# Performance work log

Hardware: AMD Instinct MI355X
Metric: run time of the kernel (lower is better)

The kernel has to match this reference:

```python
import jax, jax.numpy as jnp
import numpy as np

EPS = 1e-5


def _batchnorm(x, gamma, beta):
    # training-mode batch norm over the node axis, per feature channel
    mean = jnp.mean(x, axis=0)
    var = jnp.var(x, axis=0)  # biased variance, as torch uses for normalization
    return (x - mean) * jax.lax.rsqrt(var + EPS) * gamma + beta


def _gcn_conv(h, W, b, src, dst, norm, n_nodes):
    # h: [N, Fin] -> [N, Fout]; D^{-1/2}(A+I)D^{-1/2} (h W) + b
    h = h @ W                                   # [N, Fout]
    msgs = h[src] * norm[:, None]               # [E+N, Fout] gathered, normalized
    out = jax.ops.segment_sum(msgs, dst, num_segments=n_nodes)
    return out + b


def setup_inputs() -> dict:
    key = jax.random.key(0)
    ks = jax.random.split(key, 8)
    N, F, E, H = 50000, 512, 800000, 256
    inp = {
        "x": jax.random.normal(ks[0], (N, F), jnp.float32),
        "edge_index": jax.random.randint(ks[1], (2, E), 0, N, jnp.int64),
        "gamma1": jnp.ones((F,), jnp.float32),
        "beta1": jnp.zeros((F,), jnp.float32),
        "W1": jax.random.normal(ks[2], (F, H), jnp.float32) * (1.0 / np.sqrt(F)),
        "b1": jnp.zeros((H,), jnp.float32),
        "W2": jax.random.normal(ks[3], (H, H), jnp.float32) * (1.0 / np.sqrt(H)),
        "b2": jnp.zeros((H,), jnp.float32),
        "W3": jax.random.normal(ks[4], (H, H), jnp.float32) * (1.0 / np.sqrt(H)),
        "b3": jnp.zeros((H,), jnp.float32),
        "W4": jax.random.normal(ks[5], (H, H), jnp.float32) * (1.0 / np.sqrt(H)),
        "b4": jnp.zeros((H,), jnp.float32),
        "gamma2": jnp.ones((H,), jnp.float32),
        "beta2": jnp.zeros((H,), jnp.float32),
        "Wd": jax.random.normal(ks[6], (H, 5), jnp.float32) * (1.0 / np.sqrt(H)),
        "bd": jnp.zeros((5,), jnp.float32),
    }
    return inp


def reference(x, edge_index, gamma1, beta1, W1, b1, W2, b2, W3, b3, W4, b4,
              gamma2, beta2, Wd, bd):
    N = x.shape[0]
    loops = jnp.arange(N, dtype=edge_index.dtype)
    src = jnp.concatenate([edge_index[0], loops])
    dst = jnp.concatenate([edge_index[1], loops])
    deg = jax.ops.segment_sum(jnp.ones_like(src, dtype=x.dtype), dst, num_segments=N)
    dinv = jax.lax.rsqrt(deg)                    # deg >= 1 due to self-loops
    norm = dinv[src] * dinv[dst]                 # [E+N]

    h = _batchnorm(x, gamma1, beta1)
    h = _gcn_conv(h, W1, b1, src, dst, norm, N)
    h = _gcn_conv(h, W2, b2, src, dst, norm, N)
    h = _gcn_conv(h, W3, b3, src, dst, norm, N)
    h = _gcn_conv(h, W4, b4, src, dst, norm, N)
    h = _batchnorm(h, gamma2, beta2)
    # Flatten(start_dim=1) is identity on [N, 256]
    return jax.nn.sigmoid(h @ Wd + bd)           # [N, 5]
```

## Files before the change

kernel.cpp:

```cpp
#include <hip/hip_runtime.h>
#include <math.h>

#define BN_EPS 1e-5f

typedef float floatx4 __attribute__((ext_vector_type(4)));
typedef short shortx4 __attribute__((ext_vector_type(4)));
typedef short shortx8 __attribute__((ext_vector_type(8)));
typedef __bf16 bf16x8 __attribute__((ext_vector_type(8)));

__device__ __forceinline__ unsigned short f2b(float f) {
    unsigned int u = __builtin_bit_cast(unsigned int, f);
    u += 0x7fffu + ((u >> 16) & 1u);
    return (unsigned short)(u >> 16);
}
__device__ __forceinline__ float b2f(unsigned short s) {
    unsigned int u = ((unsigned int)s) << 16;
    return __builtin_bit_cast(float, u);
}
__device__ __forceinline__ float b2f_s(short s) { return b2f((unsigned short)s); }

__global__ __launch_bounds__(256)
void k_detect(const unsigned int* __restrict__ ei, int n_check, int* __restrict__ flag) {
    __shared__ int any;
    if (threadIdx.x == 0) any = 0;
    __syncthreads();
    for (int i = threadIdx.x; i < n_check; i += 256) {
        if (ei[2 * i + 1] != 0u) any = 1;
    }
    __syncthreads();
    if (threadIdx.x == 0) *flag = any;
}

__global__ __launch_bounds__(256)
void k_convert(const void* __restrict__ ei_raw, const int* __restrict__ flag,
               int* __restrict__ src, int* __restrict__ dst, int* __restrict__ cnt, int E) {
    int e = blockIdx.x * 256 + threadIdx.x;
    if (e >= E) return;
    int s, d;
    if (*flag) {
        const int* a = (const int*)ei_raw;
        s = a[e]; d = a[E + e];
    } else {
        const long long* a = (const long long*)ei_raw;
        s = (int)a[e]; d = (int)a[E + e];
    }
    src[e] = s;
    dst[e] = d;
    atomicAdd(&cnt[d], 1);
}

__global__ __launch_bounds__(1024)
void k_scan_sum(const int* __restrict__ cnt, int* __restrict__ bsum, int N) {
    __shared__ int s[1024];
    int i = blockIdx.x * 1024 + threadIdx.x;
    s[threadIdx.x] = (i < N) ? cnt[i] : 0;
    __syncthreads();
    for (int off = 512; off > 0; off >>= 1) {
        if (threadIdx.x < off) s[threadIdx.x] += s[threadIdx.x + off];
        __syncthreads();
    }
    if (threadIdx.x == 0) bsum[blockIdx.x] = s[0];
}

__global__ __launch_bounds__(1024)
void k_scan_part(int* __restrict__ bsum, int nb) {
    __shared__ int s[1024];
    int t = threadIdx.x;
    int v = (t < nb) ? bsum[t] : 0;
    s[t] = v;
    __syncthreads();
    for (int off = 1; off < 1024; off <<= 1) {
        int tmp = (t >= off) ? s[t - off] : 0;
        __syncthreads();
        s[t] += tmp;
        __syncthreads();
    }
    if (t < nb) bsum[t] = s[t] - v;
}

__global__ __launch_bounds__(1024)
void k_scan_final(const int* __restrict__ cnt, const int* __restrict__ bsum,
                  int* __restrict__ row_ptr, int* __restrict__ cursor,
                  float* __restrict__ dinv, int N) {
    __shared__ int s[1024];
    int b = blockIdx.x, t = threadIdx.x;
    int i = b * 1024 + t;
    int v = (i < N) ? cnt[i] : 0;
    s[t] = v;
    __syncthreads();
    for (int off = 1; off < 1024; off <<= 1) {
        int tmp = (t >= off) ? s[t - off] : 0;
        __syncthreads();
        s[t] += tmp;
        __syncthreads();
    }
    if (i < N) {
        int excl = bsum[b] + s[t] - v;
        row_ptr[i] = excl;
        cursor[i]  = excl;
        dinv[i] = rsqrtf((float)(v + 1));
        if (i == N - 1) row_ptr[N] = excl + v;
    }
}

__global__ __launch_bounds__(256)
void k_fill(const int* __restrict__ src, const int* __restrict__ dst,
            int* __restrict__ cursor, const float* __restrict__ dinv,
            int2* __restrict__ csr_sw, int E) {
    int e = blockIdx.x * 256 + threadIdx.x;
    if (e >= E) return;
    int s = src[e], d = dst[e];
    int p = atomicAdd(&cursor[d], 1);
    float w = dinv[s] * dinv[d];
    csr_sw[p] = make_int2(s, __builtin_bit_cast(int, w));
}

__global__ __launch_bounds__(256)
void k_bnstats_cast(const float* __restrict__ x, unsigned short* __restrict__ xb,
                    float* __restrict__ sum8, float* __restrict__ sumsq8, int N, int F) {
    __shared__ float ls[512], lq[512];
    int q   = F >> 2;
    int t   = threadIdx.x;
    int cq  = t % q;
    int ro  = t / q;
    int rpp = 256 / q;
    int step = gridDim.x * rpp;
    float s0 = 0.f, s1 = 0.f, s2 = 0.f, s3 = 0.f;
    float q0 = 0.f, q1 = 0.f, q2 = 0.f, q3 = 0.f;
    size_t colb = (size_t)cq * 4;
    for (int r = blockIdx.x * rpp + ro; r < N; r += 4 * step) {
        int rb = r + step, rc = r + 2 * step, rd = r + 3 * step;
        bool ob = rb < N, oc = rc < N, od = rd < N;
        float4 va = *(const float4*)&x[(size_t)r * F + colb];
        float4 vb, vc, vd;
        if (ob) vb = *(const float4*)&x[(size_t)rb * F + colb];
        if (oc) vc = *(const float4*)&x[(size_t)rc * F + colb];
        if (od) vd = *(const float4*)&x[(size_t)rd * F + colb];
        shortx4 o;
        o[0] = (short)f2b(va.x); o[1] = (short)f2b(va.y);
        o[2] = (short)f2b(va.z); o[3] = (short)f2b(va.w);
        *(shortx4*)&xb[(size_t)r * F + colb] = o;
        s0 += va.x; s1 += va.y; s2 += va.z; s3 += va.w;
        q0 += va.x * va.x; q1 += va.y * va.y; q2 += va.z * va.z; q3 += va.w * va.w;
        if (ob) {
            o[0] = (short)f2b(vb.x); o[1] = (short)f2b(vb.y);
            o[2] = (short)f2b(vb.z); o[3] = (short)f2b(vb.w);
            *(shortx4*)&xb[(size_t)rb * F + colb] = o;
            s0 += vb.x; s1 += vb.y; s2 += vb.z; s3 += vb.w;
            q0 += vb.x * vb.x; q1 += vb.y * vb.y; q2 += vb.z * vb.z; q3 += vb.w * vb.w;
        }
        if (oc) {
            o[0] = (short)f2b(vc.x); o[1] = (short)f2b(vc.y);
            o[2] = (short)f2b(vc.z); o[3] = (short)f2b(vc.w);
            *(shortx4*)&xb[(size_t)rc * F + colb] = o;
            s0 += vc.x; s1 += vc.y; s2 += vc.z; s3 += vc.w;
            q0 += vc.x * vc.x; q1 += vc.y * vc.y; q2 += vc.z * vc.z; q3 += vc.w * vc.w;
        }
        if (od) {
            o[0] = (short)f2b(vd.x); o[1] = (short)f2b(vd.y);
            o[2] = (short)f2b(vd.z); o[3] = (short)f2b(vd.w);
            *(shortx4*)&xb[(size_t)rd * F + colb] = o;
            s0 += vd.x; s1 += vd.y; s2 += vd.z; s3 += vd.w;
            q0 += vd.x * vd.x; q1 += vd.y * vd.y; q2 += vd.z * vd.z; q3 += vd.w * vd.w;
        }
    }
    for (int c = t; c < F; c += 256) { ls[c] = 0.f; lq[c] = 0.f; }
    __syncthreads();
    atomicAdd(&ls[cq * 4 + 0], s0); atomicAdd(&ls[cq * 4 + 1], s1);
    atomicAdd(&ls[cq * 4 + 2], s2); atomicAdd(&ls[cq * 4 + 3], s3);
    atomicAdd(&lq[cq * 4 + 0], q0); atomicAdd(&lq[cq * 4 + 1], q1);
    atomicAdd(&lq[cq * 4 + 2], q2); atomicAdd(&lq[cq * 4 + 3], q3);
    __syncthreads();
    int rep = (blockIdx.x & 7) * F;
    for (int c = t; c < F; c += 256) {
        atomicAdd(&sum8[rep + c],   ls[c]);
        atomicAdd(&sumsq8[rep + c], lq[c]);
    }
}

__global__ __launch_bounds__(256)
void k_bnstats_b(const unsigned short* __restrict__ x, float* __restrict__ sum,
                 float* __restrict__ sumsq, int N, int H) {
    __shared__ float ls[256], lq[256];
    int t  = threadIdx.x;
    int cg = t & 31;
    int ro = t >> 5;
    int step = gridDim.x * 8;
    float s[8], q[8];
    #pragma unroll
    for (int j = 0; j < 8; ++j) { s[j] = 0.f; q[j] = 0.f; }
    for (int r = blockIdx.x * 8 + ro; r < N; r += step) {
        shortx8 v = *(const shortx8*)&x[(size_t)r * H + cg * 8];
        #pragma unroll
        for (int j = 0; j < 8; ++j) {
            float f = b2f_s(v[j]);
            s[j] += f; q[j] += f * f;
        }
    }
    ls[t] = 0.f; lq[t] = 0.f;
    __syncthreads();
    #pragma unroll
    for (int j = 0; j < 8; ++j) {
        atomicAdd(&ls[cg * 8 + j], s[j]);
        atomicAdd(&lq[cg * 8 + j], q[j]);
    }
    __syncthreads();
    int rep = (blockIdx.x & 3) * H;
    atomicAdd(&sum[rep + t],   ls[t]);
    atomicAdd(&sumsq[rep + t], lq[t]);
}

__global__ __launch_bounds__(256)
void k_bnfin(const float* __restrict__ sum, const float* __restrict__ sumsq,
             const float* __restrict__ gamma, const float* __restrict__ beta,
             float* __restrict__ a, float* __restrict__ b, int N, int F, int nrep) {
    int c = blockIdx.x * 256 + threadIdx.x;
    if (c >= F) return;
    float s = 0.f, ss = 0.f;
    for (int i = 0; i < nrep; ++i) { s += sum[i * F + c]; ss += sumsq[i * F + c]; }
    float m   = s / (float)N;
    float var = ss / (float)N - m * m;
    float rs  = rsqrtf(var + BN_EPS);
    float aa  = gamma[c] * rs;
    a[c] = aa;
    b[c] = beta[c] - m * aa;
}

__global__ __launch_bounds__(256)
void k_castWT4(const float* __restrict__ W1, const float* __restrict__ W2,
               const float* __restrict__ W3, const float* __restrict__ W4,
               unsigned short* __restrict__ T1, unsigned short* __restrict__ T2,
               unsigned short* __restrict__ T3, unsigned short* __restrict__ T4,
               const float* __restrict__ bna, int F, int H) {
    int i = blockIdx.x * 256 + threadIdx.x;
    int n1 = F * H, n2 = H * H;
    if (i < n1) {
        int n = i / F, k = i % F;
        T1[i] = f2b(W1[(size_t)k * H + n] * bna[k]);
        return;
    }
    const float* W; unsigned short* T; int j;
    if (i < n1 + n2)          { W = W2; T = T2; j = i - n1; }
    else if (i < n1 + 2 * n2) { W = W3; T = T3; j = i - n1 - n2; }
    else if (i < n1 + 3 * n2) { W = W4; T = T4; j = i - n1 - 2 * n2; }
    else return;
    int n = j / H, k = j % H;
    T[j] = f2b(W[(size_t)k * H + n]);
}

__global__ __launch_bounds__(256)
void k_cvec(const float* __restrict__ W1, const float* __restrict__ bnb,
            float* __restrict__ cvec, int F, int H) {
    int j = threadIdx.x;
    int kslice = F / 8;
    int k0 = blockIdx.x * kslice;
    float s = 0.f;
    for (int k = k0; k < k0 + kslice; ++k)
        s += bnb[k] * W1[(size_t)k * H + j];
    atomicAdd(&cvec[j], s);
}

__device__ __forceinline__ void glds16(const void* g, void* l) {
    __builtin_amdgcn_global_load_lds(
        (const __attribute__((address_space(1))) unsigned int*)g,
        (__attribute__((address_space(3))) unsigned int*)l, 16, 0, 0);
}

__global__ __launch_bounds__(256)
void k_gemm_bf16(const unsigned short* __restrict__ A, const unsigned short* __restrict__ Bt,
                 unsigned short* __restrict__ C, int K, int NC) {
    __shared__ unsigned short As[128 * 32];
    __shared__ unsigned short Bs[128 * 32];
    int tid  = threadIdx.x;
    int wave = tid >> 6, lane = tid & 63;
    int row0 = blockIdx.x * 128;
    int col0 = blockIdx.y * 128;
    int wr = (wave & 1) * 64;
    int wc = (wave >> 1) * 64;

    floatx4 acc[4][4];
    #pragma unroll
    for (int i = 0; i < 4; i++)
        #pragma unroll
        for (int j = 0; j < 4; j++) acc[i][j] = (floatx4){0.f, 0.f, 0.f, 0.f};

    int cA = tid * 16;
    int cB = cA + 4096;
    const char* Ab = (const char*)A;
    const char* Bb = (const char*)Bt;
    size_t a_off0 = (size_t)(row0 + (cA >> 6)) * K * 2 + (cA & 63);
    size_t a_off1 = (size_t)(row0 + (cB >> 6)) * K * 2 + (cB & 63);
    size_t b_off0 = (size_t)(col0 + (cA >> 6)) * K * 2 + (cA & 63);
    size_t b_off1 = (size_t)(col0 + (cB >> 6)) * K * 2 + (cB & 63);

    int lm  = lane & 15;
    int lk8 = (lane >> 4) * 8;

    for (int ks = 0; ks < K; ks += 32) {
        size_t koff = (size_t)ks * 2;
        glds16(Ab + a_off0 + koff, (char*)As + cA);
        glds16(Ab + a_off1 + koff, (char*)As + cA + 4096);
        glds16(Bb + b_off0 + koff, (char*)Bs + cA);
        glds16(Bb + b_off1 + koff, (char*)Bs + cA + 4096);
        __syncthreads();

        bf16x8 af[4], bfr[4];
        #pragma unroll
        for (int i = 0; i < 4; i++) {
            shortx8 s = *(const shortx8*)&As[(wr + i * 16 + lm) * 32 + lk8];
            af[i] = __builtin_bit_cast(bf16x8, s);
        }
        #pragma unroll
        for (int j = 0; j < 4; j++) {
            shortx8 s = *(const shortx8*)&Bs[(wc + j * 16 + lm) * 32 + lk8];
            bfr[j] = __builtin_bit_cast(bf16x8, s);
        }
        #pragma unroll
        for (int i = 0; i < 4; i++)
            #pragma unroll
            for (int j = 0; j < 4; j++)
                acc[i][j] = __builtin_amdgcn_mfma_f32_16x16x32_bf16(af[i], bfr[j], acc[i][j], 0, 0, 0);
        __syncthreads();
    }

    int crow = row0 + wr + (lane >> 4) * 4;
    int ccol = col0 + wc + lm;
    #pragma unroll
    for (int i = 0; i < 4; i++)
        #pragma unroll
        for (int j = 0; j < 4; j++)
            #pragma unroll
            for (int r = 0; r < 4; r++)
                C[(size_t)(crow + i * 16 + r) * NC + ccol + j * 16] = f2b(acc[i][j][r]);
}

__global__ __launch_bounds__(256)
void k_agg(const unsigned short* __restrict__ hin, unsigned short* __restrict__ hout,
           const int* __restrict__ row_ptr, const int2* __restrict__ csr_sw,
           const float* __restrict__ dinv, const float* __restrict__ bias,
           const float* __restrict__ cvec, int N) {
    const int H = 256;
    int node = blockIdx.x * 4 + (threadIdx.x >> 6);
    if (node >= N) return;
    int lane = threadIdx.x & 63;
    int half = lane >> 5;
    int f = (lane & 31) * 8;
    float acc[8];
    float ws;
    float di = dinv[node];
    if (half == 0) {
        shortx8 hv = *(const shortx8*)&hin[(size_t)node * H + f];
        float sl = di * di;
        ws = sl;
        #pragma unroll
        for (int j = 0; j < 8; ++j) acc[j] = b2f_s(hv[j]) * sl;
    } else {
        ws = 0.f;
        #pragma unroll
        for (int j = 0; j < 8; ++j) acc[j] = 0.f;
    }
    int e0 = row_ptr[node], e1 = row_ptr[node + 1];
    int e = e0;
    for (; e + 8 <= e1; e += 8) {
        int2 p0 = csr_sw[e + 0 + half];
        int2 p1 = csr_sw[e + 2 + half];
        int2 p2 = csr_sw[e + 4 + half];
        int2 p3 = csr_sw[e + 6 + half];
        shortx8 r0 = *(const shortx8*)&hin[(size_t)p0.x * H + f];
        shortx8 r1 = *(const shortx8*)&hin[(size_t)p1.x * H + f];
        shortx8 r2 = *(const shortx8*)&hin[(size_t)p2.x * H + f];
        shortx8 r3 = *(const shortx8*)&hin[(size_t)p3.x * H + f];
        float w0 = __builtin_bit_cast(float, p0.y);
        float w1 = __builtin_bit_cast(float, p1.y);
        float w2 = __builtin_bit_cast(float, p2.y);
        float w3 = __builtin_bit_cast(float, p3.y);
        ws += (w0 + w1) + (w2 + w3);
        #pragma unroll
        for (int j = 0; j < 8; ++j)
            acc[j] += w0 * b2f_s(r0[j]) + w1 * b2f_s(r1[j])
                    + w2 * b2f_s(r2[j]) + w3 * b2f_s(r3[j]);
    }
    for (; e < e1; e += 2) {
        int idx = e + half;
        bool valid = idx < e1;
        int2 pr = csr_sw[valid ? idx : e];
        float w = valid ? __builtin_bit_cast(float, pr.y) : 0.f;
        shortx8 r = *(const shortx8*)&hin[(size_t)pr.x * H + f];
        ws += w;
        #pragma unroll
        for (int j = 0; j < 8; ++j) acc[j] += w * b2f_s(r[j]);
    }
    #pragma unroll
    for (int j = 0; j < 8; ++j) acc[j] += __shfl_xor(acc[j], 32, 64);
    ws += __shfl_xor(ws, 32, 64);
    if (half == 0) {
        float4 bi0 = *(const float4*)&bias[f];
        float4 bi1 = *(const float4*)&bias[f + 4];
        if (cvec) {
            float4 c0 = *(const float4*)&cvec[f];
            float4 c1 = *(const float4*)&cvec[f + 4];
            bi0.x += ws * c0.x; bi0.y += ws * c0.y;
            bi0.z += ws * c0.z; bi0.w += ws * c0.w;
            bi1.x += ws * c1.x; bi1.y += ws * c1.y;
            bi1.z += ws * c1.z; bi1.w += ws * c1.w;
        }
        shortx8 o;
        o[0] = (short)f2b(acc[0] + bi0.x);
        o[1] = (short)f2b(acc[1] + bi0.y);
        o[2] = (short)f2b(acc[2] + bi0.z);
        o[3] = (short)f2b(acc[3] + bi0.w);
        o[4] = (short)f2b(acc[4] + bi1.x);
        o[5] = (short)f2b(acc[5] + bi1.y);
        o[6] = (short)f2b(acc[6] + bi1.z);
        o[7] = (short)f2b(acc[7] + bi1.w);
        *(shortx8*)&hout[(size_t)node * H + f] = o;
    }
}

__global__ __launch_bounds__(256)
void k_head(const unsigned short* __restrict__ h, const float* __restrict__ a,
            const float* __restrict__ b, const float* __restrict__ Wd,
            const float* __restrict__ bd, float* __restrict__ out, int N) {
    int node = blockIdx.x * 4 + (threadIdx.x >> 6);
    if (node >= N) return;
    int lane = threadIdx.x & 63;
    int f = lane * 4;
    shortx4 hv = *(const shortx4*)&h[(size_t)node * 256 + f];
    float v0 = b2f_s(hv[0]) * a[f + 0] + b[f + 0];
    float v1 = b2f_s(hv[1]) * a[f + 1] + b[f + 1];
    float v2 = b2f_s(hv[2]) * a[f + 2] + b[f + 2];
    float v3 = b2f_s(hv[3]) * a[f + 3] + b[f + 3];
    float s[5];
    #pragma unroll
    for (int j = 0; j < 5; ++j) {
        s[j] = v0 * Wd[(f + 0) * 5 + j] + v1 * Wd[(f + 1) * 5 + j] +
               v2 * Wd[(f + 2) * 5 + j] + v3 * Wd[(f + 3) * 5 + j];
    }
    #pragma unroll
    for (int off = 32; off > 0; off >>= 1) {
        #pragma unroll
        for (int j = 0; j < 5; ++j) s[j] += __shfl_down(s[j], off, 64);
    }
    if (lane == 0) {
        #pragma unroll
        for (int j = 0; j < 5; ++j) {
            float z = s[j] + bd[j];
            out[(size_t)node * 5 + j] = 1.f / (1.f + expf(-z));
        }
    }
}

extern "C" void kernel_launch(void* const* d_in, const int* in_sizes, int n_in,
                              void* d_out, int out_size, void* d_ws, size_t ws_size,
                              hipStream_t stream) {
    const float* x      = (const float*)d_in[0];
    const void*  ei_raw = d_in[1];
    const float* gamma1 = (const float*)d_in[2];
    const float* beta1  = (const float*)d_in[3];
    const float* W1 = (const float*)d_in[4];
    const float* b1 = (const float*)d_in[5];
    const float* W2 = (const float*)d_in[6];
    const float* b2 = (const float*)d_in[7];
    const float* W3 = (const float*)d_in[8];
    const float* b3 = (const float*)d_in[9];
    const float* W4 = (const float*)d_in[10];
    const float* b4 = (const float*)d_in[11];
    const float* gamma2 = (const float*)d_in[12];
    const float* beta2  = (const float*)d_in[13];
    const float* Wd = (const float*)d_in[14];
    const float* bd = (const float*)d_in[15];

    const int F = in_sizes[2];
    const int N = in_sizes[0] / F;
    const int E = in_sizes[1] / 2;
    const int H = in_sizes[5];
    const int Mpad = ((N + 127) / 128) * 128;
    const int NB   = (N + 1023) / 1024;
    float* out = (float*)d_out;

    char* p = (char*)d_ws;
    auto alloc = [&](size_t bytes) {
        void* r = (void*)p;
        p += (bytes + 255) & ~(size_t)255;
        return r;
    };
    int*   flag    = (int*)  alloc(4);
    int*   srcA    = (int*)  alloc((size_t)E * 4);
    int*   dstA    = (int*)  alloc((size_t)E * 4);
    char*  zstart  = p;
    int*   cnt     = (int*)  alloc((size_t)N * 4);
    float* colsum8 = (float*)alloc((size_t)8 * F * 4);
    float* colsq8  = (float*)alloc((size_t)8 * F * 4);
    float* colsum2 = (float*)alloc((size_t)4 * H * 4);
    float* colsq2  = (float*)alloc((size_t)4 * H * 4);
    float* cvec    = (float*)alloc((size_t)H * 4);
    size_t zbytes  = (size_t)(p - zstart);
    int*   row_ptr = (int*)  alloc(((size_t)N + 1) * 4);
    int*   cursor  = (int*)  alloc((size_t)N * 4);
    float* dinv    = (float*)alloc((size_t)N * 4);
    int2*  csr_sw  = (int2*) alloc((size_t)E * 8);
    int*   bsum    = (int*)  alloc((size_t)NB * 4);
    float* bna     = (float*)alloc((size_t)F * 4);
    float* bnb     = (float*)alloc((size_t)F * 4);
    unsigned short* W1t = (unsigned short*)alloc((size_t)F * H * 2);
    unsigned short* W2t = (unsigned short*)alloc((size_t)H * H * 2);
    unsigned short* W3t = (unsigned short*)alloc((size_t)H * H * 2);
    unsigned short* W4t = (unsigned short*)alloc((size_t)H * H * 2);
    unsigned short* xb  = (unsigned short*)alloc((size_t)Mpad * F * 2);
    unsigned short* hbA = (unsigned short*)alloc((size_t)Mpad * H * 2);
    unsigned short* hbB = (unsigned short*)alloc((size_t)Mpad * H * 2);

    hipMemsetAsync(zstart, 0, zbytes, stream);
    hipMemsetAsync(xb + (size_t)N * F, 0, (size_t)(Mpad - N) * F * 2, stream);

    int n_check = (E >= 2048) ? 2048 : E;
    k_detect<<<1, 256, 0, stream>>>((const unsigned int*)ei_raw, n_check, flag);
    k_convert<<<(E + 255) / 256, 256, 0, stream>>>(ei_raw, flag, srcA, dstA, cnt, E);
    k_scan_sum<<<NB, 1024, 0, stream>>>(cnt, bsum, N);
    k_scan_part<<<1, 1024, 0, stream>>>(bsum, NB);
    k_scan_final<<<NB, 1024, 0, stream>>>(cnt, bsum, row_ptr, cursor, dinv, N);
    k_fill<<<(E + 255) / 256, 256, 0, stream>>>(srcA, dstA, cursor, dinv, csr_sw, E);

    k_bnstats_cast<<<2048, 256, 0, stream>>>(x, xb, colsum8, colsq8, N, F);
    k_bnfin<<<(F + 255) / 256, 256, 0, stream>>>(colsum8, colsq8, gamma1, beta1, bna, bnb, N, F, 8);

    int tot = F * H + 3 * H * H;
    k_castWT4<<<(tot + 255) / 256, 256, 0, stream>>>(W1, W2, W3, W4, W1t, W2t, W3t, W4t, bna, F, H);
    k_cvec<<<8, 256, 0, stream>>>(W1, bnb, cvec, F, H);

    dim3 gg(Mpad / 128, H / 128);
    int aggb = (N + 3) / 4;
    k_gemm_bf16<<<gg, 256, 0, stream>>>(xb, W1t, hbA, F, H);
    k_agg<<<aggb, 256, 0, stream>>>(hbA, hbB, row_ptr, csr_sw, dinv, b1, cvec, N);
    k_gemm_bf16<<<gg, 256, 0, stream>>>(hbB, W2t, hbA, H, H);
    k_agg<<<aggb, 256, 0, stream>>>(hbA, hbB, row_ptr, csr_sw, dinv, b2, nullptr, N);
    k_gemm_bf16<<<gg, 256, 0, stream>>>(hbB, W3t, hbA, H, H);
    k_agg<<<aggb, 256, 0, stream>>>(hbA, hbB, row_ptr, csr_sw, dinv, b3, nullptr, N);
    k_gemm_bf16<<<gg, 256, 0, stream>>>(hbB, W4t, hbA, H, H);
    k_agg<<<aggb, 256, 0, stream>>>(hbA, hbB, row_ptr, csr_sw, dinv, b4, nullptr, N);

    k_bnstats_b<<<1024, 256, 0, stream>>>(hbB, colsum2, colsq2, N, H);
    k_bnfin<<<(H + 255) / 256, 256, 0, stream>>>(colsum2, colsq2, gamma2, beta2, bna, bnb, N, H, 4);
    k_head<<<(N + 3) / 4, 256, 0, stream>>>(hbB, bna, bnb, Wd, bd, out, N);
}
```

Measured before the change: 693.4 us.

## Drop edge staging arrays, fuse weight prep, vectorize GEMM stores, deepen agg gather

The edge conversion kernel no longer writes src/dst staging arrays. A count kernel reads the raw edge index for degrees, and the fill kernel rereads the raw index directly. The weight cast and cvec kernels are merged into one launch. The GEMM swaps its MFMA operands so each lane holds four consecutive columns and writes them as one 8-byte vector store instead of scalar stores. The aggregation loop now issues 8 neighbor gathers per half-wave per iteration instead of 4, with vectorized tails, for more memory-level parallelism at the cost of more registers.

```diff
diff --git a/kernel.cpp b/kernel.cpp
--- a/kernel.cpp
+++ b/kernel.cpp
@@ -32,8 +32,73 @@
 }
 
 __global__ __launch_bounds__(256)
-void k_convert(const void* __restrict__ ei_raw, const int* __restrict__ flag,
-               int* __restrict__ src, int* __restrict__ dst, int* __restrict__ cnt, int E) {
+void k_count(const void* __restrict__ ei_raw, const int* __restrict__ flag,
+             int* __restrict__ cnt, int E) {
+    int e = blockIdx.x * 256 + threadIdx.x;
+    if (e >= E) return;
+    int d = (*flag) ? ((const int*)ei_raw)[E + e]
+                    : (int)((const long long*)ei_raw)[E + e];
+    atomicAdd(&cnt[d], 1);
+}
+
+__global__ __launch_bounds__(1024)
+void k_scan_sum(const int* __restrict__ cnt, int* __restrict__ bsum, int N) {
+    __shared__ int s[1024];
+    int i = blockIdx.x * 1024 + threadIdx.x;
+    s[threadIdx.x] = (i < N) ? cnt[i] : 0;
+    __syncthreads();
+    for (int off = 512; off > 0; off >>= 1) {
+        if (threadIdx.x < off) s[threadIdx.x] += s[threadIdx.x + off];
+        __syncthreads();
+    }
+    if (threadIdx.x == 0) bsum[blockIdx.x] = s[0];
+}
+
+__global__ __launch_bounds__(1024)
+void k_scan_part(int* __restrict__ bsum, int nb) {
+    __shared__ int s[1024];
+    int t = threadIdx.x;
+    int v = (t < nb) ? bsum[t] : 0;
+    s[t] = v;
+    __syncthreads();
+    for (int off = 1; off < 1024; off <<= 1) {
+        int tmp = (t >= off) ? s[t - off] : 0;
+        __syncthreads();
+        s[t] += tmp;
+        __syncthreads();
+    }
+    if (t < nb) bsum[t] = s[t] - v;
+}
+
+__global__ __launch_bounds__(1024)
+void k_scan_final(const int* __restrict__ cnt, const int* __restrict__ bsum,
+                  int* __restrict__ row_ptr, int* __restrict__ cursor,
+                  float* __restrict__ dinv, int N) {
+    __shared__ int s[1024];
+    int b = blockIdx.x, t = threadIdx.x;
+    int i = b * 1024 + t;
+    int v = (i < N) ? cnt[i] : 0;
+    s[t] = v;
+    __syncthreads();
+    for (int off = 1; off < 1024; off <<= 1) {
+        int tmp = (t >= off) ? s[t - off] : 0;
+        __syncthreads();
+        s[t] += tmp;
+        __syncthreads();
+    }
+    if (i < N) {
+        int excl = bsum[b] + s[t] - v;
+        row_ptr[i] = excl;
+        cursor[i]  = excl;
+        dinv[i] = rsqrtf((float)(v + 1));
+        if (i == N - 1) row_ptr[N] = excl + v;
+    }
+}
+
+__global__ __launch_bounds__(256)
+void k_fill(const void* __restrict__ ei_raw, const int* __restrict__ flag,
+            int* __restrict__ cursor, const float* __restrict__ dinv,
+            int2* __restrict__ csr_sw, int E) {
     int e = blockIdx.x * 256 + threadIdx.x;
     if (e >= E) return;
     int s, d;
@@ -44,72 +109,6 @@
         const long long* a = (const long long*)ei_raw;
         s = (int)a[e]; d = (int)a[E + e];
     }
-    src[e] = s;
-    dst[e] = d;
-    atomicAdd(&cnt[d], 1);
-}
-
-__global__ __launch_bounds__(1024)
-void k_scan_sum(const int* __restrict__ cnt, int* __restrict__ bsum, int N) {
-    __shared__ int s[1024];
-    int i = blockIdx.x * 1024 + threadIdx.x;
-    s[threadIdx.x] = (i < N) ? cnt[i] : 0;
-    __syncthreads();
-    for (int off = 512; off > 0; off >>= 1) {
-        if (threadIdx.x < off) s[threadIdx.x] += s[threadIdx.x + off];
-        __syncthreads();
-    }
-    if (threadIdx.x == 0) bsum[blockIdx.x] = s[0];
-}
-
-__global__ __launch_bounds__(1024)
-void k_scan_part(int* __restrict__ bsum, int nb) {
-    __shared__ int s[1024];
-    int t = threadIdx.x;
-    int v = (t < nb) ? bsum[t] : 0;
-    s[t] = v;
-    __syncthreads();
-    for (int off = 1; off < 1024; off <<= 1) {
-        int tmp = (t >= off) ? s[t - off] : 0;
-        __syncthreads();
-        s[t] += tmp;
-        __syncthreads();
-    }
-    if (t < nb) bsum[t] = s[t] - v;
-}
-
-__global__ __launch_bounds__(1024)
-void k_scan_final(const int* __restrict__ cnt, const int* __restrict__ bsum,
-                  int* __restrict__ row_ptr, int* __restrict__ cursor,
-                  float* __restrict__ dinv, int N) {
-    __shared__ int s[1024];
-    int b = blockIdx.x, t = threadIdx.x;
-    int i = b * 1024 + t;
-    int v = (i < N) ? cnt[i] : 0;
-    s[t] = v;
-    __syncthreads();
-    for (int off = 1; off < 1024; off <<= 1) {
-        int tmp = (t >= off) ? s[t - off] : 0;
-        __syncthreads();
-        s[t] += tmp;
-        __syncthreads();
-    }
-    if (i < N) {
-        int excl = bsum[b] + s[t] - v;
-        row_ptr[i] = excl;
-        cursor[i]  = excl;
-        dinv[i] = rsqrtf((float)(v + 1));
-        if (i == N - 1) row_ptr[N] = excl + v;
-    }
-}
-
-__global__ __launch_bounds__(256)
-void k_fill(const int* __restrict__ src, const int* __restrict__ dst,
-            int* __restrict__ cursor, const float* __restrict__ dinv,
-            int2* __restrict__ csr_sw, int E) {
-    int e = blockIdx.x * 256 + threadIdx.x;
-    if (e >= E) return;
-    int s = src[e], d = dst[e];
     int p = atomicAdd(&cursor[d], 1);
     float w = dinv[s] * dinv[d];
     csr_sw[p] = make_int2(s, __builtin_bit_cast(int, w));
@@ -227,11 +226,23 @@
 }
 
 __global__ __launch_bounds__(256)
-void k_castWT4(const float* __restrict__ W1, const float* __restrict__ W2,
-               const float* __restrict__ W3, const float* __restrict__ W4,
-               unsigned short* __restrict__ T1, unsigned short* __restrict__ T2,
-               unsigned short* __restrict__ T3, unsigned short* __restrict__ T4,
-               const float* __restrict__ bna, int F, int H) {
+void k_prep_w(const float* __restrict__ W1, const float* __restrict__ W2,
+              const float* __restrict__ W3, const float* __restrict__ W4,
+              unsigned short* __restrict__ T1, unsigned short* __restrict__ T2,
+              unsigned short* __restrict__ T3, unsigned short* __restrict__ T4,
+              const float* __restrict__ bna, const float* __restrict__ bnb,
+              float* __restrict__ cvec, int F, int H, int wblocks) {
+    if ((int)blockIdx.x >= wblocks) {
+        int bi = blockIdx.x - wblocks;
+        int j = threadIdx.x;
+        int kslice = F / 8;
+        int k0 = bi * kslice;
+        float s = 0.f;
+        for (int k = k0; k < k0 + kslice; ++k)
+            s += bnb[k] * W1[(size_t)k * H + j];
+        atomicAdd(&cvec[j], s);
+        return;
+    }
     int i = blockIdx.x * 256 + threadIdx.x;
     int n1 = F * H, n2 = H * H;
     if (i < n1) {
@@ -246,18 +257,6 @@
     else return;
     int n = j / H, k = j % H;
     T[j] = f2b(W[(size_t)k * H + n]);
-}
-
-__global__ __launch_bounds__(256)
-void k_cvec(const float* __restrict__ W1, const float* __restrict__ bnb,
-            float* __restrict__ cvec, int F, int H) {
-    int j = threadIdx.x;
-    int kslice = F / 8;
-    int k0 = blockIdx.x * kslice;
-    float s = 0.f;
-    for (int k = k0; k < k0 + kslice; ++k)
-        s += bnb[k] * W1[(size_t)k * H + j];
-    atomicAdd(&cvec[j], s);
 }
 
 __device__ __forceinline__ void glds16(const void* g, void* l) {
@@ -319,19 +318,26 @@
         for (int i = 0; i < 4; i++)
             #pragma unroll
             for (int j = 0; j < 4; j++)
-                acc[i][j] = __builtin_amdgcn_mfma_f32_16x16x32_bf16(af[i], bfr[j], acc[i][j], 0, 0, 0);
-        __syncthreads();
-    }
-
-    int crow = row0 + wr + (lane >> 4) * 4;
-    int ccol = col0 + wc + lm;
-    #pragma unroll
-    for (int i = 0; i < 4; i++)
-        #pragma unroll
-        for (int j = 0; j < 4; j++)
-            #pragma unroll
-            for (int r = 0; r < 4; r++)
-                C[(size_t)(crow + i * 16 + r) * NC + ccol + j * 16] = f2b(acc[i][j][r]);
+                acc[i][j] = __builtin_amdgcn_mfma_f32_16x16x32_bf16(bfr[j], af[i], acc[i][j], 0, 0, 0);
+        __syncthreads();
+    }
+
+    int quad = lane >> 4;
+    int crow0 = row0 + wr + lm;
+    int ccol0 = col0 + wc + quad * 4;
+    #pragma unroll
+    for (int i = 0; i < 4; i++) {
+        size_t rbase = (size_t)(crow0 + i * 16) * NC;
+        #pragma unroll
+        for (int j = 0; j < 4; j++) {
+            shortx4 o;
+            o[0] = (short)f2b(acc[i][j][0]);
+            o[1] = (short)f2b(acc[i][j][1]);
+            o[2] = (short)f2b(acc[i][j][2]);
+            o[3] = (short)f2b(acc[i][j][3]);
+            *(shortx4*)&C[rbase + ccol0 + j * 16] = o;
+        }
+    }
 }
 
 __global__ __launch_bounds__(256)
@@ -345,9 +351,10 @@
     int lane = threadIdx.x & 63;
     int half = lane >> 5;
     int f = (lane & 31) * 8;
+    int e0 = row_ptr[node], e1 = row_ptr[node + 1];
+    float di = dinv[node];
     float acc[8];
     float ws;
-    float di = dinv[node];
     if (half == 0) {
         shortx8 hv = *(const shortx8*)&hin[(size_t)node * H + f];
         float sl = di * di;
@@ -359,36 +366,59 @@
         #pragma unroll
         for (int j = 0; j < 8; ++j) acc[j] = 0.f;
     }
-    int e0 = row_ptr[node], e1 = row_ptr[node + 1];
     int e = e0;
-    for (; e + 8 <= e1; e += 8) {
-        int2 p0 = csr_sw[e + 0 + half];
-        int2 p1 = csr_sw[e + 2 + half];
-        int2 p2 = csr_sw[e + 4 + half];
-        int2 p3 = csr_sw[e + 6 + half];
-        shortx8 r0 = *(const shortx8*)&hin[(size_t)p0.x * H + f];
-        shortx8 r1 = *(const shortx8*)&hin[(size_t)p1.x * H + f];
-        shortx8 r2 = *(const shortx8*)&hin[(size_t)p2.x * H + f];
-        shortx8 r3 = *(const shortx8*)&hin[(size_t)p3.x * H + f];
-        float w0 = __builtin_bit_cast(float, p0.y);
-        float w1 = __builtin_bit_cast(float, p1.y);
-        float w2 = __builtin_bit_cast(float, p2.y);
-        float w3 = __builtin_bit_cast(float, p3.y);
-        ws += (w0 + w1) + (w2 + w3);
-        #pragma unroll
-        for (int j = 0; j < 8; ++j)
-            acc[j] += w0 * b2f_s(r0[j]) + w1 * b2f_s(r1[j])
-                    + w2 * b2f_s(r2[j]) + w3 * b2f_s(r3[j]);
-    }
-    for (; e < e1; e += 2) {
-        int idx = e + half;
-        bool valid = idx < e1;
-        int2 pr = csr_sw[valid ? idx : e];
-        float w = valid ? __builtin_bit_cast(float, pr.y) : 0.f;
-        shortx8 r = *(const shortx8*)&hin[(size_t)pr.x * H + f];
-        ws += w;
-        #pragma unroll
-        for (int j = 0; j < 8; ++j) acc[j] += w * b2f_s(r[j]);
+    for (; e + 16 <= e1; e += 16) {
+        int2 pp[8];
+        #pragma unroll
+        for (int k = 0; k < 8; ++k) pp[k] = csr_sw[e + 2 * k + half];
+        shortx8 rr[8];
+        #pragma unroll
+        for (int k = 0; k < 8; ++k)
+            rr[k] = *(const shortx8*)&hin[(size_t)pp[k].x * H + f];
+        #pragma unroll
+        for (int k = 0; k < 8; ++k) {
+            float w = __builtin_bit_cast(float, pp[k].y);
+            ws += w;
+            #pragma unroll
+            for (int j = 0; j < 8; ++j) acc[j] += w * b2f_s(rr[k][j]);
+        }
+    }
+    if (e + 8 <= e1) {
+        int2 pp[4];
+        #pragma unroll
+        for (int k = 0; k < 4; ++k) pp[k] = csr_sw[e + 2 * k + half];
+        shortx8 rr[4];
+        #pragma unroll
+        for (int k = 0; k < 4; ++k)
+            rr[k] = *(const shortx8*)&hin[(size_t)pp[k].x * H + f];
+        #pragma unroll
+        for (int k = 0; k < 4; ++k) {
+            float w = __builtin_bit_cast(float, pp[k].y);
+            ws += w;
+            #pragma unroll
+            for (int j = 0; j < 8; ++j) acc[j] += w * b2f_s(rr[k][j]);
+        }
+        e += 8;
+    }
+    if (e < e1) {
+        int2 pp[4]; float wv[4];
+        #pragma unroll
+        for (int k = 0; k < 4; ++k) {
+            int idx = e + 2 * k + half;
+            bool v = idx < e1;
+            pp[k] = csr_sw[v ? idx : e];
+            wv[k] = v ? __builtin_bit_cast(float, pp[k].y) : 0.f;
+        }
+        shortx8 rr[4];
+        #pragma unroll
+        for (int k = 0; k < 4; ++k)
+            rr[k] = *(const shortx8*)&hin[(size_t)pp[k].x * H + f];
+        #pragma unroll
+        for (int k = 0; k < 4; ++k) {
+            ws += wv[k];
+            #pragma unroll
+            for (int j = 0; j < 8; ++j) acc[j] += wv[k] * b2f_s(rr[k][j]);
+        }
     }
     #pragma unroll
     for (int j = 0; j < 8; ++j) acc[j] += __shfl_xor(acc[j], 32, 64);
@@ -485,8 +515,6 @@
         return r;
     };
     int*   flag    = (int*)  alloc(4);
-    int*   srcA    = (int*)  alloc((size_t)E * 4);
-    int*   dstA    = (int*)  alloc((size_t)E * 4);
     char*  zstart  = p;
     int*   cnt     = (int*)  alloc((size_t)N * 4);
     float* colsum8 = (float*)alloc((size_t)8 * F * 4);
@@ -515,18 +543,19 @@
 
     int n_check = (E >= 2048) ? 2048 : E;
     k_detect<<<1, 256, 0, stream>>>((const unsigned int*)ei_raw, n_check, flag);
-    k_convert<<<(E + 255) / 256, 256, 0, stream>>>(ei_raw, flag, srcA, dstA, cnt, E);
+    k_count<<<(E + 255) / 256, 256, 0, stream>>>(ei_raw, flag, cnt, E);
     k_scan_sum<<<NB, 1024, 0, stream>>>(cnt, bsum, N);
     k_scan_part<<<1, 1024, 0, stream>>>(bsum, NB);
     k_scan_final<<<NB, 1024, 0, stream>>>(cnt, bsum, row_ptr, cursor, dinv, N);
-    k_fill<<<(E + 255) / 256, 256, 0, stream>>>(srcA, dstA, cursor, dinv, csr_sw, E);
+    k_fill<<<(E + 255) / 256, 256, 0, stream>>>(ei_raw, flag, cursor, dinv, csr_sw, E);
 
     k_bnstats_cast<<<2048, 256, 0, stream>>>(x, xb, colsum8, colsq8, N, F);
     k_bnfin<<<(F + 255) / 256, 256, 0, stream>>>(colsum8, colsq8, gamma1, beta1, bna, bnb, N, F, 8);
 
     int tot = F * H + 3 * H * H;
-    k_castWT4<<<(tot + 255) / 256, 256, 0, stream>>>(W1, W2, W3, W4, W1t, W2t, W3t, W4t, bna, F, H);
-    k_cvec<<<8, 256, 0, stream>>>(W1, bnb, cvec, F, H);
+    int wblocks = (tot + 255) / 256;
+    k_prep_w<<<wblocks + 8, 256, 0, stream>>>(W1, W2, W3, W4, W1t, W2t, W3t, W4t,
+                                              bna, bnb, cvec, F, H, wblocks);
 
     dim3 gg(Mpad / 128, H / 128);
     int aggb = (N + 3) / 4;
```

Result: slower. 712.4 us (+2.7%).
